# Kernel optimization log

Measured on AMD Instinct MI355X. Metric: run time of the kernel, lower is better.

Reference implementation:

```python
import jax, jax.numpy as jnp
import numpy as np

H = 450    # hidden_size (JTNN default)
LAT = 56   # latent_size (tree_vec dim)
V = 780    # vocab size
T = 1024   # n_trees
L = 24     # nodes per tree (path topology)


def _tree_meta(Ln):
    # forward edge i: (i, i+1) eid=i ; reverse edge i: (i+1, i) eid=(Ln-1)+i
    n_f = Ln - 1
    eids, preds, srcs, dsts, labels = [], [], [], [], []
    for i in range(n_f):  # forward DFS steps
        eids.append(i); srcs.append(i); dsts.append(i + 1)
        preds.append(i - 1 if i > 0 else -1); labels.append(0)
    for k in range(n_f):  # backtrack DFS steps (reverse edges, deepest first)
        i = n_f - 1 - k
        eids.append(n_f + i); srcs.append(i + 1); dsts.append(i)
        preds.append(n_f + i + 1 if i < n_f - 1 else -1); labels.append(1)
    # incoming edges of the dst node v (for the node 'pull' h = sum of m)
    in1 = [d - 1 if d > 0 else -1 for d in dsts]
    in2 = [n_f + d if d < n_f else -1 for d in dsts]
    meta = [np.asarray(a, np.int32) for a in (eids, preds, srcs, dsts, in1, in2)]
    return meta, np.asarray(labels, np.float32)


def setup_inputs():
    key = jax.random.key(0)
    ks = jax.random.split(key, 12)
    s = 0.05
    return {
        "wid": jax.random.randint(ks[0], (T, L), 0, V, dtype=jnp.int32),
        "tree_vec": jax.random.normal(ks[1], (T, LAT), jnp.float32),
        "emb": jax.random.normal(ks[2], (V, H)) * s,
        "W_w": jax.random.normal(ks[3], (H + LAT, H)) * s, "W_b": jnp.zeros((H,)),
        "U_w": jax.random.normal(ks[4], (2 * H + LAT, H)) * s, "U_b": jnp.zeros((H,)),
        "Wo_w": jax.random.normal(ks[5], (H, V)) * s, "Wo_b": jnp.zeros((V,)),
        "Us_w": jax.random.normal(ks[6], (H, 1)) * s, "Us_b": jnp.zeros((1,)),
        "Wz_w": jax.random.normal(ks[7], (2 * H, H)) * s, "Wz_b": jnp.zeros((H,)),
        "Wr_w": jax.random.normal(ks[8], (H, H)) * s,
        "Ur_w": jax.random.normal(ks[9], (H, H)) * s, "Ur_b": jnp.zeros((H,)),
        "Wh_w": jax.random.normal(ks[10], (2 * H, H)) * s, "Wh_b": jnp.zeros((H,)),
    }


def reference(wid, tree_vec, emb, W_w, W_b, U_w, U_b, Wo_w, Wo_b, Us_w, Us_b,
              Wz_w, Wz_b, Wr_w, Ur_w, Ur_b, Wh_w, Wh_b):
    Tn, Ln = wid.shape
    n_f = Ln - 1
    nE = 2 * n_f
    meta, labels = _tree_meta(Ln)
    xs = tuple(jnp.asarray(a) for a in meta)
    x = emb[wid]                                  # [T, L, H] node features
    m0 = jnp.zeros((Tn, nE, H), x.dtype)
    rm0 = jnp.zeros((Tn, nE, H), x.dtype)

    def step(carry, sx_):
        m, rm = carry
        eid, pred, src, dst, i1, i2 = sx_
        gp = jnp.maximum(pred, 0)
        s = jnp.where(pred >= 0, m[:, gp], 0.0)        # line-graph pull: sum of m
        arm = jnp.where(pred >= 0, rm[:, gp], 0.0)     # accum_rm
        sxn = x[:, src]                                # src_x
        dxn = x[:, dst]                                # dst_x
        z = jax.nn.sigmoid(jnp.concatenate([sxn, s], 1) @ Wz_w + Wz_b)
        mt = jnp.tanh(jnp.concatenate([sxn, arm], 1) @ Wh_w + Wh_b)
        m_new = (1.0 - z) * s + z * mt
        r = jax.nn.sigmoid(dxn @ Wr_w + m_new @ Ur_w + Ur_b)
        m = m.at[:, eid].set(m_new)
        rm = rm.at[:, eid].set(r * m_new)
        # node pull on v: h_v = sum of m over incoming edges (post edge update)
        h_v = (jnp.where(i1 >= 0, m[:, jnp.maximum(i1, 0)], 0.0)
               + jnp.where(i2 >= 0, m[:, jnp.maximum(i2, 0)], 0.0))
        return (m, rm), (h_v, dxn)

    (_, _), (hs, xvs) = jax.lax.scan(step, (m0, rm0), xs)  # [nE, T, H] each

    tv_steps = jnp.broadcast_to(tree_vec, (nE, Tn, LAT))
    p_in = jnp.concatenate([
        jnp.concatenate([x[:, 0], jnp.zeros((Tn, H), x.dtype), tree_vec], 1),
        jnp.concatenate([xvs, hs, tv_steps], -1).reshape(-1, 2 * H + LAT),
    ], 0)
    q_in = jnp.concatenate([
        jnp.concatenate([jnp.zeros((Tn, H), x.dtype), tree_vec], 1),
        jnp.concatenate([hs[:n_f], tv_steps[:n_f]], -1).reshape(-1, H + LAT),
    ], 0)
    p_targets = jnp.concatenate([jnp.repeat(jnp.asarray(1.0 - labels), Tn),
                                 jnp.zeros((Tn,), jnp.float32)])
    q_targets = wid.T.reshape(-1)

    q_logits = jax.nn.relu(q_in @ W_w + W_b) @ Wo_w + Wo_b
    p_logit = (jax.nn.relu(p_in @ U_w + U_b) @ Us_w + Us_b)[:, 0]
    p_loss = jnp.sum(p_targets * jax.nn.softplus(-p_logit)
                     + (1.0 - p_targets) * jax.nn.softplus(p_logit)) / Tn
    logp = jax.nn.log_softmax(q_logits, -1)
    q_loss = -jnp.sum(jnp.take_along_axis(logp, q_targets[:, None], 1)) / Tn
    p_acc = jnp.mean(((p_logit > 0).astype(jnp.int32) == p_targets.astype(jnp.int32)).astype(jnp.float32))
    q_acc = jnp.mean((jnp.argmax(q_logits, 1) == q_targets).astype(jnp.float32))
    return (q_loss, p_loss, q_acc, p_acc)
```

## Files before the change

### kernel.cpp

```cpp
#include <hip/hip_runtime.h>
#include <hip/hip_bf16.h>
#include <math.h>

#define H 450
#define HP 464
#define KP 480
#define LAT 56
#define V 780
#define LW 24
#define NE 46
#define NF 23
#define SLOT (1024*HP)
#define SROWS 2048
#define QROWS (24*1024)
#define PROWS (47*1024)
#define PTGT  (23*1024)
#define QBLK 6144
#define XBSZ ((size_t)QROWS * H)

typedef __hip_bfloat16 bf16;
typedef __attribute__((ext_vector_type(8))) short short8;
typedef __attribute__((ext_vector_type(4))) float f32x4;

#define MFMA16(a,b,c) __builtin_amdgcn_mfma_f32_16x16x32_bf16(a,b,c,0,0,0)

__device__ __forceinline__ float sigm(float x) { return 1.f / (1.f + expf(-x)); }
__device__ __forceinline__ float toF(bf16 x) { return __bfloat162float(x); }
__device__ __forceinline__ void stV(float* p, float v) { *p = v; }
__device__ __forceinline__ void stV(bf16* p, float v) { *p = __float2bfloat16(v); }
__device__ __forceinline__ short8 ld8(const bf16* p) { return *reinterpret_cast<const short8*>(p); }

__device__ __forceinline__ void gl_lds(const bf16* g, bf16* l) {
    __builtin_amdgcn_global_load_lds(
        (const __attribute__((address_space(1))) void*)g,
        (__attribute__((address_space(3))) void*)l, 16, 0, 0);
}

__device__ __forceinline__ void xcd_decode128(int b, int C, int& row0, int& col0) {
    int rres = b & 7;
    int colt = (b >> 3) % C;
    int g    = b / (8 * C);
    row0 = (rres + 8 * g) * 128;
    col0 = colt * 128;
}

__global__ __launch_bounds__(256)
void make_bt(const float* __restrict__ src, int K, int N, int ld,
             bf16* __restrict__ dst, int npad) {
    int idx = blockIdx.x * 256 + threadIdx.x;
    if (idx >= npad * KP) return;
    int n = idx / KP, k = idx - n * KP;
    float v = (n < N && k < K) ? src[(size_t)k * ld + n] : 0.f;
    dst[idx] = __float2bfloat16(v);
}

__global__ __launch_bounds__(256)
void pack_bias(const float* __restrict__ zb, const float* __restrict__ hb,
               const float* __restrict__ rb, float* __restrict__ bias4) {
    int i = blockIdx.x * 256 + threadIdx.x;
    if (i >= 1856) return;
    float v = 0.f;
    if (i < 450)       v = zb[i];
    else if (i < 900)  v = hb[i - 450];
    else if (i < 1350) v = rb[i - 900];
    bias4[i] = v;
}

__global__ __launch_bounds__(256)
void zero_init(float* __restrict__ out) {
    int i = threadIdx.x;
    if (i < 4) out[i] = 0.f;
}

__global__ __launch_bounds__(256)
void gather_x(const float* __restrict__ emb, const int* __restrict__ wid,
              bf16* __restrict__ x_all) {
    int e = blockIdx.x * 256 + threadIdx.x;
    if (e >= 24 * 1024 * 225) return;
    int row = e / 225, h2 = e - row * 225;
    int t = row >> 10, n = row & 1023;
    int v = wid[n * LW + t];
    float2 x = ((const float2*)(emb + (size_t)v * H))[h2];
    bf16* dst = x_all + (size_t)row * HP + 2 * h2;
    dst[0] = __float2bfloat16(x.x);
    dst[1] = __float2bfloat16(x.y);
}

template<typename TC>
__global__ __launch_bounds__(256)
void gemm128(const bf16* __restrict__ A, int lda,
             const bf16* __restrict__ Bt, int N, int cblk,
             TC* __restrict__ C, int ldc,
             const float* __restrict__ bias,
             const float* __restrict__ addrow, int addld, int relu) {
    __shared__ bf16 As[128 * 32];
    __shared__ bf16 Bs[128 * 32];
    int tid = threadIdx.x;
    int lane = tid & 63, wave = tid >> 6;
    int wx = wave & 1, wy = wave >> 1;
    int lrow = lane & 15, quad = lane >> 4;
    int perm = ((quad + (lrow >> 1)) & 3) * 8;
    int row0, col0;
    xcd_decode128(blockIdx.x, cblk, row0, col0);
    f32x4 acc[4][4] = {};
    for (int k0i = 0; k0i < 15; k0i++) {
        int k0 = k0i * 32;
#pragma unroll
        for (int r = 0; r < 2; r++) {
            int tt = r * 256 + tid;
            int row = tt >> 2, cl = tt & 3;
            int cg = (cl - (row >> 1)) & 3;
            gl_lds(A  + (size_t)(row0 + row) * lda + k0 + cg * 8, As + tt * 8);
            gl_lds(Bt + (size_t)(col0 + row) * KP  + k0 + cg * 8, Bs + tt * 8);
        }
        __syncthreads();
        short8 a[4], b[4];
#pragma unroll
        for (int f = 0; f < 4; f++)
            a[f] = ld8(As + (wy * 64 + f * 16 + lrow) * 32 + perm);
#pragma unroll
        for (int f = 0; f < 4; f++)
            b[f] = ld8(Bs + (wx * 64 + f * 16 + lrow) * 32 + perm);
#pragma unroll
        for (int fi = 0; fi < 4; fi++)
#pragma unroll
            for (int fj = 0; fj < 4; fj++)
                acc[fi][fj] = MFMA16(a[fi], b[fj], acc[fi][fj]);
        __syncthreads();
    }
#pragma unroll
    for (int fi = 0; fi < 4; fi++)
#pragma unroll
        for (int e = 0; e < 4; e++) {
            int r = row0 + wy * 64 + fi * 16 + quad * 4 + e;
#pragma unroll
            for (int fj = 0; fj < 4; fj++) {
                int c = col0 + wx * 64 + fj * 16 + lrow;
                if (c >= N) continue;
                float v = acc[fi][fj][e];
                if (bias) v += bias[c];
                if (addrow) v += addrow[(size_t)(r & 1023) * addld + c];
                if (relu) v = fmaxf(v, 0.f);
                stV(&C[(size_t)r * ldc + c], v);
            }
        }
}

__global__ __launch_bounds__(256)
void gemm128_pre(const bf16* __restrict__ A,
                 const bf16* __restrict__ Bt,
                 bf16* __restrict__ X0,
                 const float* __restrict__ bias4) {
    __shared__ bf16 As[128 * 32];
    __shared__ bf16 Bs[128 * 32];
    int tid = threadIdx.x;
    int lane = tid & 63, wave = tid >> 6;
    int wx = wave & 1, wy = wave >> 1;
    int lrow = lane & 15, quad = lane >> 4;
    int perm = ((quad + (lrow >> 1)) & 3) * 8;
    int row0, col0;
    xcd_decode128(blockIdx.x, 15, row0, col0);
    f32x4 acc[4][4] = {};
    for (int k0i = 0; k0i < 15; k0i++) {
        int k0 = k0i * 32;
#pragma unroll
        for (int r = 0; r < 2; r++) {
            int tt = r * 256 + tid;
            int row = tt >> 2, cl = tt & 3;
            int cg = (cl - (row >> 1)) & 3;
            gl_lds(A  + (size_t)(row0 + row) * HP + k0 + cg * 8, As + tt * 8);
            gl_lds(Bt + (size_t)(col0 + row) * KP + k0 + cg * 8, Bs + tt * 8);
        }
        __syncthreads();
        short8 a[4], b[4];
#pragma unroll
        for (int f = 0; f < 4; f++)
            a[f] = ld8(As + (wy * 64 + f * 16 + lrow) * 32 + perm);
#pragma unroll
        for (int f = 0; f < 4; f++)
            b[f] = ld8(Bs + (wx * 64 + f * 16 + lrow) * 32 + perm);
#pragma unroll
        for (int fi = 0; fi < 4; fi++)
#pragma unroll
            for (int fj = 0; fj < 4; fj++)
                acc[fi][fj] = MFMA16(a[fi], b[fj], acc[fi][fj]);
        __syncthreads();
    }
#pragma unroll
    for (int fi = 0; fi < 4; fi++)
#pragma unroll
        for (int e = 0; e < 4; e++) {
            int r = row0 + wy * 64 + fi * 16 + quad * 4 + e;
#pragma unroll
            for (int fj = 0; fj < 4; fj++) {
                int c = col0 + wx * 64 + fj * 16 + lrow;
                if (c >= 1800) continue;
                int mm = c / 450;
                int cc = c - mm * 450;
                float v = acc[fi][fj][e] + bias4[c];
                X0[(size_t)mm * XBSZ + (size_t)r * H + cc] = __float2bfloat16(v);
            }
        }
}

__global__ __launch_bounds__(256)
void p_gemm128(const bf16* __restrict__ hs, const bf16* __restrict__ UbT,
               const bf16* __restrict__ XUa, const float* __restrict__ Ptv,
               const float* __restrict__ Us, float* __restrict__ pl) {
    __shared__ bf16 As[128 * 32];
    __shared__ bf16 Bs[128 * 32];
    int tid = threadIdx.x;
    int lane = tid & 63, wave = tid >> 6;
    int wx = wave & 1, wy = wave >> 1;
    int lrow = lane & 15, quad = lane >> 4;
    int perm = ((quad + (lrow >> 1)) & 3) * 8;
    int row0, col0;
    xcd_decode128(blockIdx.x, 4, row0, col0);
    f32x4 acc[4][4] = {};
    for (int k0i = 0; k0i < 15; k0i++) {
        int k0 = k0i * 32;
#pragma unroll
        for (int r = 0; r < 2; r++) {
            int tt = r * 256 + tid;
            int row = tt >> 2, cl = tt & 3;
            int cg = (cl - (row >> 1)) & 3;
            gl_lds(hs  + (size_t)(row0 + row) * HP + k0 + cg * 8, As + tt * 8);
            gl_lds(UbT + (size_t)(col0 + row) * KP + k0 + cg * 8, Bs + tt * 8);
        }
        __syncthreads();
        short8 a[4], b[4];
#pragma unroll
        for (int f = 0; f < 4; f++)
            a[f] = ld8(As + (wy * 64 + f * 16 + lrow) * 32 + perm);
#pragma unroll
        for (int f = 0; f < 4; f++)
            b[f] = ld8(Bs + (wx * 64 + f * 16 + lrow) * 32 + perm);
#pragma unroll
        for (int fi = 0; fi < 4; fi++)
#pragma unroll
            for (int fj = 0; fj < 4; fj++)
                acc[fi][fj] = MFMA16(a[fi], b[fj], acc[fi][fj]);
        __syncthreads();
    }
#pragma unroll
    for (int fi = 0; fi < 4; fi++)
#pragma unroll
        for (int e = 0; e < 4; e++) {
            int r = row0 + wy * 64 + fi * 16 + quad * 4 + e;
            int t = r >> 10, n = r & 1023;
            int dst = (t < 23) ? (t + 1) : (45 - t);
            float part = 0.f;
#pragma unroll
            for (int fj = 0; fj < 4; fj++) {
                int c = col0 + wx * 64 + fj * 16 + lrow;
                if (c < H) {
                    float h = fmaxf(acc[fi][fj][e] + toF(XUa[((size_t)dst * 1024 + n) * H + c])
                                    + Ptv[(size_t)n * H + c], 0.f);
                    part += h * Us[c];
                }
            }
#pragma unroll
            for (int off = 1; off < 16; off <<= 1)
                part += __shfl_xor(part, off);
            if (lrow == 0) atomicAdd(&pl[1024 + r], part);
        }
}

__global__ __launch_bounds__(256)
void tv_gemm(const float* __restrict__ tv, const float* __restrict__ Wlat,
             const float* __restrict__ bias, float* __restrict__ out) {
    int n = blockIdx.y;
    int c = blockIdx.x * 256 + threadIdx.x;
    __shared__ float tvs[LAT];
    if (threadIdx.x < LAT) tvs[threadIdx.x] = tv[n * LAT + threadIdx.x];
    __syncthreads();
    if (c < H) {
        float a = bias[c];
#pragma unroll 8
        for (int k = 0; k < LAT; k++) a += tvs[k] * Wlat[(size_t)k * H + c];
        out[(size_t)n * H + c] = a;
    }
}

__global__ __launch_bounds__(1024)
void scan_full(bf16* __restrict__ hs,
               const bf16* __restrict__ WzbT, const bf16* __restrict__ WhbT,
               const bf16* __restrict__ UrT,
               const bf16* __restrict__ Xz, const bf16* __restrict__ Xh,
               const bf16* __restrict__ Xr) {
    __shared__ bf16 mnl[2][16][488];
    __shared__ bf16 rml[16][488];
    int tid = threadIdx.x;
    int lane = tid & 63, w = tid >> 6;
    int lrow = lane & 15, quad = lane >> 4;
    int row0 = blockIdx.x * 16;
    bool fwd = row0 < 1024;
    int f0 = w, f1 = w + 16;
    bool hasf1 = (f1 < 29);
    float sreg[2][4];
#pragma unroll
    for (int i = 0; i < 2; i++)
#pragma unroll
        for (int e = 0; e < 4; e++) sreg[i][e] = 0.f;
    for (int i = tid; i < 2 * 16 * 488; i += 1024) ((bf16*)mnl)[i] = __float2bfloat16(0.f);
    for (int i = tid; i < 16 * 488; i += 1024) ((bf16*)rml)[i] = __float2bfloat16(0.f);
    __syncthreads();

    for (int u = 0; u < 23; u++) {
        int cur = u & 1, prev = cur ^ 1;
        f32x4 az[2], ah[2];
#pragma unroll
        for (int i = 0; i < 2; i++) {
            az[i] = (f32x4){0.f, 0.f, 0.f, 0.f};
            ah[i] = (f32x4){0.f, 0.f, 0.f, 0.f};
        }
        if (u > 0) {
            for (int k = 0; k < 15; k++) {
                short8 sA = *reinterpret_cast<const short8*>(&mnl[prev][lrow][k * 32 + quad * 8]);
                short8 rA = *reinterpret_cast<const short8*>(&rml[lrow][k * 32 + quad * 8]);
                {
                    short8 zB = ld8(WzbT + (size_t)(f0 * 16 + lrow) * KP + k * 32 + quad * 8);
                    short8 hB = ld8(WhbT + (size_t)(f0 * 16 + lrow) * KP + k * 32 + quad * 8);
                    az[0] = MFMA16(sA, zB, az[0]);
                    ah[0] = MFMA16(rA, hB, ah[0]);
                }
                if (hasf1) {
                    short8 zB = ld8(WzbT + (size_t)(f1 * 16 + lrow) * KP + k * 32 + quad * 8);
                    short8 hB = ld8(WhbT + (size_t)(f1 * 16 + lrow) * KP + k * 32 + quad * 8);
                    az[1] = MFMA16(sA, zB, az[1]);
                    ah[1] = MFMA16(rA, hB, ah[1]);
                }
            }
        }
        int src = fwd ? u : 23 - u;
        bf16* hso = hs + (size_t)(fwd ? u : 23 + u) * SLOT;
#pragma unroll
        for (int i = 0; i < 2; i++) {
            int f = (i == 0) ? f0 : f1;
            if (i == 1 && !hasf1) break;
            int c = f * 16 + lrow;
            if (c < H) {
#pragma unroll
                for (int e = 0; e < 4; e++) {
                    int rl = quad * 4 + e;
                    int n = (row0 + rl) & 1023;
                    float zp = az[i][e] + toF(Xz[((size_t)src * 1024 + n) * H + c]);
                    float hp = ah[i][e] + toF(Xh[((size_t)src * 1024 + n) * H + c]);
                    float z = sigm(zp), mt = tanhf(hp);
                    float mn = (1.f - z) * sreg[i][e] + z * mt;
                    sreg[i][e] = mn;
                    bf16 mb = __float2bfloat16(mn);
                    mnl[cur][rl][c] = mb;
                    hso[(size_t)n * HP + c] = mb;
                }
            }
        }
        __syncthreads();

        if (u < 22) {
            f32x4 ar[2];
#pragma unroll
            for (int i = 0; i < 2; i++) ar[i] = (f32x4){0.f, 0.f, 0.f, 0.f};
            for (int k = 0; k < 15; k++) {
                short8 a = *reinterpret_cast<const short8*>(&mnl[cur][lrow][k * 32 + quad * 8]);
                ar[0] = MFMA16(a, ld8(UrT + (size_t)(f0 * 16 + lrow) * KP + k * 32 + quad * 8), ar[0]);
                if (hasf1)
                    ar[1] = MFMA16(a, ld8(UrT + (size_t)(f1 * 16 + lrow) * KP + k * 32 + quad * 8), ar[1]);
            }
            int dst = fwd ? (u + 1) : (22 - u);
#pragma unroll
            for (int i = 0; i < 2; i++) {
                int f = (i == 0) ? f0 : f1;
                if (i == 1 && !hasf1) break;
                int c = f * 16 + lrow;
                if (c < H) {
#pragma unroll
                    for (int e = 0; e < 4; e++) {
                        int rl = quad * 4 + e;
                        int n = (row0 + rl) & 1023;
                        float rp = ar[i][e] + toF(Xr[((size_t)dst * 1024 + n) * H + c]);
                        rml[rl][c] = __float2bfloat16(sigm(rp) * toF(mnl[cur][rl][c]));
                    }
                }
            }
            __syncthreads();
        }
    }
}

__global__ __launch_bounds__(256)
void hv_fixup(bf16* __restrict__ hs) {
    int idx = blockIdx.x * 256 + threadIdx.x;
    if (idx >= 22 * SLOT) return;
    int tl = idx / SLOT;
    int rem = idx - tl * SLOT;
    size_t a = (size_t)(23 + tl) * SLOT + rem;
    size_t b = (size_t)(21 - tl) * SLOT + rem;
    hs[a] = __float2bfloat16(toF(hs[a]) + toF(hs[b]));
}

__global__ __launch_bounds__(256)
void q_root(const float* __restrict__ Qtv, bf16* __restrict__ qh) {
    int idx = blockIdx.x * 256 + threadIdx.x;
    if (idx >= 1024 * H) return;
    int n = idx / H, c = idx - n * H;
    qh[(size_t)n * HP + c] = __float2bfloat16(fmaxf(Qtv[idx], 0.f));
}

__global__ __launch_bounds__(256)
void q_reduce(const float* __restrict__ ql, const int* __restrict__ wid,
              float* __restrict__ qred) {
    int wave = threadIdx.x >> 6, lane = threadIdx.x & 63;
    int r = blockIdx.x * 4 + wave;
    int t = r >> 10, n = r & 1023;
    int tgt = wid[n * LW + t];
    const float4* row4 = (const float4*)(ql + (size_t)r * V);
    float m = -3.4e38f, s = 0.f; int mi = 0x7fffffff;
#pragma unroll
    for (int k = 0; k < 4; k++) {
        int c4 = lane + 64 * k;
        if (c4 < 195) {
            float4 v4 = row4[c4];
            float vv[4] = {v4.x, v4.y, v4.z, v4.w};
#pragma unroll
            for (int e = 0; e < 4; e++) {
                float v = vv[e];
                if (v > m) { s = s * __expf(m - v) + 1.f; m = v; mi = c4 * 4 + e; }
                else s += __expf(v - m);
            }
        }
    }
#pragma unroll
    for (int off = 1; off < 64; off <<= 1) {
        float m2 = __shfl_xor(m, off);
        float s2 = __shfl_xor(s, off);
        int   i2 = __shfl_xor(mi, off);
        if (m2 > m || (m2 == m && i2 < mi)) {
            s = s2 + s * __expf(m - m2);
            m = m2; mi = i2;
        } else {
            s = s + s2 * __expf(m2 - m);
        }
    }
    __shared__ float lred[4][2];
    if (lane == 0) {
        float lse = m + logf(s);
        lred[wave][0] = lse - ql[(size_t)r * V + tgt];
        lred[wave][1] = (mi == tgt) ? 1.f : 0.f;
    }
    __syncthreads();
    if (threadIdx.x == 0) {
        qred[blockIdx.x * 2]     = lred[0][0] + lred[1][0] + lred[2][0] + lred[3][0];
        qred[blockIdx.x * 2 + 1] = lred[0][1] + lred[1][1] + lred[2][1] + lred[3][1];
    }
}

__global__ __launch_bounds__(256)
void q_final(const float* __restrict__ qred, float* __restrict__ out) {
    int tid = threadIdx.x;
    float L = 0.f, A = 0.f;
    for (int i = tid; i < QBLK; i += 256) { L += qred[2 * i]; A += qred[2 * i + 1]; }
    __shared__ float s1[256], s2[256];
    s1[tid] = L; s2[tid] = A;
    __syncthreads();
    for (int k = 128; k > 0; k >>= 1) {
        if (tid < k) { s1[tid] += s1[tid + k]; s2[tid] += s2[tid + k]; }
        __syncthreads();
    }
    if (tid == 0) {
        out[0] = s1[0] * (1.f / 1024.f);
        out[2] = s2[0] * (1.f / 24576.f);
    }
}

__global__ __launch_bounds__(256)
void p_init(float* __restrict__ pl, const float* __restrict__ Us_b) {
    int idx = blockIdx.x * 256 + threadIdx.x;
    if (idx < PROWS) pl[idx] = Us_b[0];
}

__global__ __launch_bounds__(256)
void p_root(const bf16* __restrict__ XUa, const float* __restrict__ Ptv,
            const float* __restrict__ Us, float* __restrict__ pl) {
    int n = blockIdx.x;
    int tid = threadIdx.x;
    const bf16* xa = XUa + (size_t)n * H;
    const float* pt = Ptv + (size_t)n * H;
    float s = 0.f;
    for (int c = tid; c < H; c += 256)
        s += fmaxf(toF(xa[c]) + pt[c], 0.f) * Us[c];
    __shared__ float red[256];
    red[tid] = s;
    __syncthreads();
    for (int k = 128; k > 0; k >>= 1) {
        if (tid < k) red[tid] += red[tid + k];
        __syncthreads();
    }
    if (tid == 0) atomicAdd(&pl[n], red[0]);
}

__global__ __launch_bounds__(256)
void p_final(const float* __restrict__ pl, float* __restrict__ out) {
    int r = blockIdx.x * 256 + threadIdx.x;
    int tid = threadIdx.x;
    float loss = 0.f, acc = 0.f;
    if (r < PROWS) {
        float l = pl[r];
        int tgt = (r < PTGT) ? 1 : 0;
        float x = tgt ? -l : l;
        loss = fmaxf(x, 0.f) + log1pf(expf(-fabsf(x)));
        int pred = (l > 0.f) ? 1 : 0;
        acc = (pred == tgt) ? 1.f : 0.f;
    }
    __shared__ float s1[256], s2[256];
    s1[tid] = loss; s2[tid] = acc;
    __syncthreads();
    for (int k = 128; k > 0; k >>= 1) {
        if (tid < k) { s1[tid] += s1[tid + k]; s2[tid] += s2[tid + k]; }
        __syncthreads();
    }
    if (tid == 0) {
        atomicAdd(&out[1], s1[0] * (1.f / 1024.f));
        atomicAdd(&out[3], s2[0] * (1.f / 48128.f));
    }
}

extern "C" void kernel_launch(void* const* d_in, const int* in_sizes, int n_in,
                              void* d_out, int out_size, void* d_ws, size_t ws_size,
                              hipStream_t stream) {
    const int*   wid  = (const int*)  d_in[0];
    const float* tv   = (const float*)d_in[1];
    const float* emb  = (const float*)d_in[2];
    const float* W_w  = (const float*)d_in[3];
    const float* W_b  = (const float*)d_in[4];
    const float* U_w  = (const float*)d_in[5];
    const float* U_b  = (const float*)d_in[6];
    const float* Wo_w = (const float*)d_in[7];
    const float* Wo_b = (const float*)d_in[8];
    const float* Us_w = (const float*)d_in[9];
    const float* Us_b = (const float*)d_in[10];
    const float* Wz_w = (const float*)d_in[11];
    const float* Wz_b = (const float*)d_in[12];
    const float* Wr_w = (const float*)d_in[13];
    const float* Ur_w = (const float*)d_in[14];
    const float* Ur_b = (const float*)d_in[15];
    const float* Wh_w = (const float*)d_in[16];
    const float* Wh_b = (const float*)d_in[17];
    float* out = (float*)d_out;

    char* base = (char*)d_ws;
    const size_t XBb = XBSZ * 2;
    bf16*  Xz   = (bf16*)(base);
    bf16*  Xh   = (bf16*)(base + XBb);
    bf16*  Xr   = (bf16*)(base + 2 * XBb);
    bf16*  XUa  = (bf16*)(base + 3 * XBb);
    bf16*  hs   = (bf16*)(base + 4 * XBb);
    bf16*  x_all = hs;
    char*  p1   = base + 4 * XBb + (size_t)NE * SLOT * 2;
    float* Qtv  = (float*)p1;               p1 += (size_t)1024 * H * 4;
    float* Ptv  = (float*)p1;               p1 += (size_t)1024 * H * 4;
    float* pl   = (float*)p1;               p1 += (size_t)PROWS * 4;
    float* qred = (float*)p1;               p1 += (size_t)QBLK * 2 * 4;
    float* bias4 = (float*)p1;              p1 += (size_t)1856 * 4;
    bf16*  BT   = (bf16*)p1;
    bf16* BT4   = BT;
    bf16* WzbT  = BT + (size_t)1856 * KP;
    bf16* WhbT  = WzbT + (size_t)512 * KP;
    bf16* UrT   = WhbT + (size_t)512 * KP;
    bf16* UbT   = UrT  + (size_t)512 * KP;
    bf16* WtopT = UbT  + (size_t)512 * KP;
    bf16* WoT   = WtopT + (size_t)512 * KP;
    bf16*  qh = (bf16*)base;
    float* ql = (float*)(base + (size_t)QROWS * HP * 2);

    zero_init<<<1, 256, 0, stream>>>(out);
    int btg = (512 * KP + 255) / 256;
    int btg450 = (450 * KP + 255) / 256;
    make_bt<<<btg450, 256, 0, stream>>>(Wz_w, H, H, H, BT4,                        450);
    make_bt<<<btg450, 256, 0, stream>>>(Wh_w, H, H, H, BT4 + (size_t)450 * KP,     450);
    make_bt<<<btg450, 256, 0, stream>>>(Wr_w, H, H, H, BT4 + (size_t)900 * KP,     450);
    make_bt<<<(506 * KP + 255) / 256, 256, 0, stream>>>(U_w, H, H, H, BT4 + (size_t)1350 * KP, 506);
    pack_bias<<<8, 256, 0, stream>>>(Wz_b, Wh_b, Ur_b, bias4);
    make_bt<<<btg, 256, 0, stream>>>(Wz_w + 450*450,  H, H, H, WzbT, 512);
    make_bt<<<btg, 256, 0, stream>>>(Wh_w + 450*450,  H, H, H, WhbT, 512);
    make_bt<<<btg, 256, 0, stream>>>(Ur_w,            H, H, H, UrT,  512);
    make_bt<<<btg, 256, 0, stream>>>(U_w + 450*450,   H, H, H, UbT,  512);
    make_bt<<<btg, 256, 0, stream>>>(W_w,             H, H, H, WtopT, 512);
    make_bt<<<(896 * KP + 255) / 256, 256, 0, stream>>>(Wo_w, H, V, V, WoT, 896);

    gather_x<<<(24 * 1024 * 225 + 255) / 256, 256, 0, stream>>>(emb, wid, x_all);
    gemm128_pre<<<(QROWS / 128) * 15, 256, 0, stream>>>(x_all, BT4, Xz, bias4);

    tv_gemm<<<dim3(2, 1024), 256, 0, stream>>>(tv, W_w + 450*450, W_b, Qtv);
    tv_gemm<<<dim3(2, 1024), 256, 0, stream>>>(tv, U_w + 900*450, U_b, Ptv);

    scan_full<<<SROWS / 16, 1024, 0, stream>>>(hs, WzbT, WhbT, UrT, Xz, Xh, Xr);
    hv_fixup<<<(22 * SLOT + 255) / 256, 256, 0, stream>>>(hs);

    p_init<<<(PROWS + 255) / 256, 256, 0, stream>>>(pl, Us_b);
    p_root<<<1024, 256, 0, stream>>>(XUa, Ptv, Us_w, pl);
    p_gemm128<<<(PROWS - 1024) / 128 * 4, 256, 0, stream>>>(hs, UbT, XUa, Ptv, Us_w, pl);
    p_final<<<PROWS / 256, 256, 0, stream>>>(pl, out);

    q_root<<<(1024 * H + 255) / 256, 256, 0, stream>>>(Qtv, qh);
    gemm128<bf16><<<(NF * 1024 / 128) * 4, 256, 0, stream>>>(hs, HP, WtopT, H, 4,
                                                             qh + (size_t)1024 * HP, HP,
                                                             (const float*)nullptr, Qtv, H, 1);
    gemm128<float><<<(QROWS / 128) * 7, 256, 0, stream>>>(qh, HP, WoT, V, 7, ql, V,
                                                          Wo_b, (const float*)nullptr, H, 0);
    q_reduce<<<QBLK, 256, 0, stream>>>(ql, wid, qred);
    q_final<<<1, 256, 0, stream>>>(qred, out);

    (void)in_sizes; (void)n_in; (void)out_size; (void)ws_size;
}
```

Measured before the change: 1.049 ms.

## Prefetch scan gate inputs into LDS asynchronously and coalesce hidden-state stores

Pads the precomputed X gate buffers to a row stride of HP, so each row can be copied with 16-byte global_load_lds. At each scan step the Xz/Xh/Xr tiles for the block are loaded asynchronously into shared memory, overlapping with the recurrent MFMAs, in place of scattered per-element global reads. The hidden-state output is written as coalesced float4 rows from LDS instead of strided 2-byte stores, and tanh/sigmoid switch to __expf-based fast approximations. The cost is extra LDS use and a slight loss of precision in the gates.

```diff
diff --git a/kernel.cpp b/kernel.cpp
--- a/kernel.cpp
+++ b/kernel.cpp
@@ -16,7 +16,7 @@
 #define PROWS (47*1024)
 #define PTGT  (23*1024)
 #define QBLK 6144
-#define XBSZ ((size_t)QROWS * H)
+#define XBSZ ((size_t)QROWS * HP)
 
 typedef __hip_bfloat16 bf16;
 typedef __attribute__((ext_vector_type(8))) short short8;
@@ -24,7 +24,8 @@
 
 #define MFMA16(a,b,c) __builtin_amdgcn_mfma_f32_16x16x32_bf16(a,b,c,0,0,0)
 
-__device__ __forceinline__ float sigm(float x) { return 1.f / (1.f + expf(-x)); }
+__device__ __forceinline__ float sigm(float x) { return 1.f / (1.f + __expf(-x)); }
+__device__ __forceinline__ float tanh_f(float x) { return 2.f / (1.f + __expf(-2.f * x)) - 1.f; }
 __device__ __forceinline__ float toF(bf16 x) { return __bfloat162float(x); }
 __device__ __forceinline__ void stV(float* p, float v) { *p = v; }
 __device__ __forceinline__ void stV(bf16* p, float v) { *p = __float2bfloat16(v); }
@@ -198,7 +199,7 @@
                 int mm = c / 450;
                 int cc = c - mm * 450;
                 float v = acc[fi][fj][e] + bias4[c];
-                X0[(size_t)mm * XBSZ + (size_t)r * H + cc] = __float2bfloat16(v);
+                X0[(size_t)mm * XBSZ + (size_t)r * HP + cc] = __float2bfloat16(v);
             }
         }
 }
@@ -254,7 +255,7 @@
             for (int fj = 0; fj < 4; fj++) {
                 int c = col0 + wx * 64 + fj * 16 + lrow;
                 if (c < H) {
-                    float h = fmaxf(acc[fi][fj][e] + toF(XUa[((size_t)dst * 1024 + n) * H + c])
+                    float h = fmaxf(acc[fi][fj][e] + toF(XUa[((size_t)dst * 1024 + n) * HP + c])
                                     + Ptv[(size_t)n * H + c], 0.f);
                     part += h * Us[c];
                 }
@@ -290,13 +291,19 @@
                const bf16* __restrict__ Xr) {
     __shared__ bf16 mnl[2][16][488];
     __shared__ bf16 rml[16][488];
+    __shared__ bf16 xzs[16][464];
+    __shared__ bf16 xhs[16][464];
+    __shared__ bf16 xrs[16][464];
     int tid = threadIdx.x;
     int lane = tid & 63, w = tid >> 6;
     int lrow = lane & 15, quad = lane >> 4;
     int row0 = blockIdx.x * 16;
     bool fwd = row0 < 1024;
+    int nb = row0 & 1023;
     int f0 = w, f1 = w + 16;
     bool hasf1 = (f1 < 29);
+    int crow = tid / 58, cj = tid - crow * 58;
+    bool cok = tid < 928;
     float sreg[2][4];
 #pragma unroll
     for (int i = 0; i < 2; i++)
@@ -308,6 +315,14 @@
 
     for (int u = 0; u < 23; u++) {
         int cur = u & 1, prev = cur ^ 1;
+        int src = fwd ? u : 23 - u;
+        int dst = fwd ? (u + 1) : (22 - u);
+        if (cok) {
+            gl_lds(Xz + ((size_t)src * 1024 + nb + crow) * HP + cj * 8, &xzs[0][0] + tid * 8);
+            gl_lds(Xh + ((size_t)src * 1024 + nb + crow) * HP + cj * 8, &xhs[0][0] + tid * 8);
+            if (u < 22)
+                gl_lds(Xr + ((size_t)dst * 1024 + nb + crow) * HP + cj * 8, &xrs[0][0] + tid * 8);
+        }
         f32x4 az[2], ah[2];
 #pragma unroll
         for (int i = 0; i < 2; i++) {
@@ -332,8 +347,8 @@
                 }
             }
         }
-        int src = fwd ? u : 23 - u;
-        bf16* hso = hs + (size_t)(fwd ? u : 23 + u) * SLOT;
+        __syncthreads();
+
 #pragma unroll
         for (int i = 0; i < 2; i++) {
             int f = (i == 0) ? f0 : f1;
@@ -343,19 +358,24 @@
 #pragma unroll
                 for (int e = 0; e < 4; e++) {
                     int rl = quad * 4 + e;
-                    int n = (row0 + rl) & 1023;
-                    float zp = az[i][e] + toF(Xz[((size_t)src * 1024 + n) * H + c]);
-                    float hp = ah[i][e] + toF(Xh[((size_t)src * 1024 + n) * H + c]);
-                    float z = sigm(zp), mt = tanhf(hp);
+                    float zp = az[i][e] + toF(xzs[rl][c]);
+                    float hp = ah[i][e] + toF(xhs[rl][c]);
+                    float z = sigm(zp), mt = tanh_f(hp);
                     float mn = (1.f - z) * sreg[i][e] + z * mt;
                     sreg[i][e] = mn;
-                    bf16 mb = __float2bfloat16(mn);
-                    mnl[cur][rl][c] = mb;
-                    hso[(size_t)n * HP + c] = mb;
+                    mnl[cur][rl][c] = __float2bfloat16(mn);
                 }
             }
         }
         __syncthreads();
+
+        {
+            bf16* hso = hs + (size_t)(fwd ? u : 23 + u) * SLOT;
+            if (cok) {
+                float4 v = *reinterpret_cast<const float4*>(&mnl[cur][crow][cj * 8]);
+                *reinterpret_cast<float4*>(hso + (size_t)(nb + crow) * HP + cj * 8) = v;
+            }
+        }
 
         if (u < 22) {
             f32x4 ar[2];
@@ -367,7 +387,6 @@
                 if (hasf1)
                     ar[1] = MFMA16(a, ld8(UrT + (size_t)(f1 * 16 + lrow) * KP + k * 32 + quad * 8), ar[1]);
             }
-            int dst = fwd ? (u + 1) : (22 - u);
 #pragma unroll
             for (int i = 0; i < 2; i++) {
                 int f = (i == 0) ? f0 : f1;
@@ -377,8 +396,7 @@
 #pragma unroll
                     for (int e = 0; e < 4; e++) {
                         int rl = quad * 4 + e;
-                        int n = (row0 + rl) & 1023;
-                        float rp = ar[i][e] + toF(Xr[((size_t)dst * 1024 + n) * H + c]);
+                        float rp = ar[i][e] + toF(xrs[rl][c]);
                         rml[rl][c] = __float2bfloat16(sigm(rp) * toF(mnl[cur][rl][c]));
                     }
                 }
@@ -484,7 +502,7 @@
             const float* __restrict__ Us, float* __restrict__ pl) {
     int n = blockIdx.x;
     int tid = threadIdx.x;
-    const bf16* xa = XUa + (size_t)n * H;
+    const bf16* xa = XUa + (size_t)n * HP;
     const float* pt = Ptv + (size_t)n * H;
     float s = 0.f;
     for (int c = tid; c < H; c += 256)
```

Measured after the change: 1.167 ms. 11.2% more time.
